# Performance work log

Measured on AMD Instinct MI355X. Metric: run time of the kernel, lower is better.

Reference implementation:

```python
import jax, jax.numpy as jnp
import numpy as np

N_NODES = 100000
N_EDGES = 3200000
NUM_FEAT = 14
DIM = 16
K_HOPS = 2


def setup_inputs() -> dict:
    key = jax.random.key(0)
    k1, k2, k3, k4 = jax.random.split(key, 4)
    x = jax.random.normal(k1, (N_NODES, NUM_FEAT), dtype=jnp.float32)
    edge_index = jax.random.randint(k2, (2, N_EDGES), 0, N_NODES, dtype=jnp.int64)
    # SGConv's final Linear(num_feat, dim): weight [dim, num_feat], bias [dim]
    W = jax.random.normal(k3, (DIM, NUM_FEAT), dtype=jnp.float32) / np.sqrt(NUM_FEAT)
    b = jax.random.normal(k4, (DIM,), dtype=jnp.float32) * 0.01
    return {"x": x, "edge_index": edge_index, "W": W, "b": b}


def reference(x, edge_index, W, b):
    N = x.shape[0]
    # gcn_norm: add self loops, symmetric degree normalization
    loops = jnp.arange(N, dtype=edge_index.dtype)
    row = jnp.concatenate([edge_index[0], loops])  # source nodes
    col = jnp.concatenate([edge_index[1], loops])  # destination nodes
    ones = jnp.ones(row.shape[0], dtype=x.dtype)
    deg = jax.ops.segment_sum(ones, col, num_segments=N)
    dinv = jnp.where(deg > 0, jax.lax.rsqrt(deg), 0.0)
    norm = dinv[row] * dinv[col]  # [E + N]
    # K-hop propagation: x <- (D^-1/2 (A+I) D^-1/2) x, repeated K times
    for _ in range(K_HOPS):
        x = jax.ops.segment_sum(norm[:, None] * x[row], col, num_segments=N)
    # final linear
    return x @ W.T + b
```

## Files before the change

### kernel.cpp

```cpp
#include <hip/hip_runtime.h>
#include <hip/hip_fp16.h>

#define NF 14
#define DIMOUT 16
#define BSH 9
#define NPBKT 512
#define NBKT 256
#define C1 4096
#define GSUB 8

__device__ __forceinline__ bool detect64(const int* e32) {
    bool is64 = true;
#pragma unroll
    for (int i = 1; i < 64; i += 2) is64 &= (e32[i] == 0);
    return is64;
}

__global__ __launch_bounds__(256) void k_lhist(const void* __restrict__ edges,
                                               int* __restrict__ lhistT, int E, int NBLK) {
    __shared__ int h[NBKT];
    const int t = threadIdx.x;
    h[t] = 0;
    __syncthreads();
    const int* e32 = (const int*)edges;
    const long long* e64 = (const long long*)edges;
    const bool is64 = detect64(e32);
    const int base = blockIdx.x * C1;
    const int cnt = min(C1, E - base);
    if (is64) {
        const longlong2* p2 = (const longlong2*)(e64 + (size_t)E + base);
        for (int j = 2 * t; j < cnt; j += 512) {
            longlong2 v = p2[j >> 1];
            atomicAdd(&h[((int)v.x) >> BSH], 1);
            atomicAdd(&h[((int)v.y) >> BSH], 1);
        }
    } else {
        const int2* p2 = (const int2*)(e32 + (size_t)E + base);
        for (int j = 2 * t; j < cnt; j += 512) {
            int2 v = p2[j >> 1];
            atomicAdd(&h[v.x >> BSH], 1);
            atomicAdd(&h[v.y >> BSH], 1);
        }
    }
    __syncthreads();
    lhistT[(size_t)t * NBLK + blockIdx.x] = h[t];
}

__global__ __launch_bounds__(256) void k_cscan(const int* __restrict__ lhistT,
                                               int* __restrict__ lbase,
                                               int* __restrict__ btot, int NBLK) {
    const int b = blockIdx.x;
    const int t = threadIdx.x;
    const int IPT = (NBLK + 255) / 256;
    int v[8];
    int s = 0;
    for (int k = 0; k < IPT; ++k) {
        int j = t * IPT + k;
        int x = (j < NBLK) ? lhistT[(size_t)b * NBLK + j] : 0;
        v[k] = x;
        s += x;
    }
    __shared__ int sm[256];
    sm[t] = s;
    __syncthreads();
    for (int d = 1; d < 256; d <<= 1) {
        int u = (t >= d) ? sm[t - d] : 0;
        __syncthreads();
        sm[t] += u;
        __syncthreads();
    }
    int run = sm[t] - s;
    for (int k = 0; k < IPT; ++k) {
        int j = t * IPT + k;
        if (j < NBLK) {
            lbase[(size_t)b * NBLK + j] = run;
            run += v[k];
        }
    }
    if (t == 255) btot[b] = sm[255];
}

__global__ __launch_bounds__(NBKT) void k_gscan(const int* __restrict__ btot,
                                                int* __restrict__ gregion) {
    __shared__ int sm[NBKT];
    int t = threadIdx.x;
    int v = btot[t];
    sm[t] = v;
    __syncthreads();
    for (int d = 1; d < NBKT; d <<= 1) {
        int u = (t >= d) ? sm[t - d] : 0;
        __syncthreads();
        sm[t] += u;
        __syncthreads();
    }
    gregion[t] = sm[t] - v;
    if (t == NBKT - 1) gregion[NBKT] = sm[t];
}

__global__ __launch_bounds__(256) void k_scatter(const void* __restrict__ edges,
                                                 const int* __restrict__ gregion,
                                                 const int* __restrict__ lbase,
                                                 unsigned int* __restrict__ pairs,
                                                 int E, int NBLK) {
    __shared__ unsigned int raw[C1];
    __shared__ unsigned int srt[C1];
    __shared__ unsigned short bkt[C1];
    __shared__ unsigned char sbk[C1];
    __shared__ int hist[NBKT], scn[NBKT], gb[NBKT], cur[NBKT];
    const int* e32 = (const int*)edges;
    const long long* e64 = (const long long*)edges;
    const bool is64 = detect64(e32);
    const int t = threadIdx.x;
    const int base = blockIdx.x * C1;
    const int cnt = min(C1, E - base);
    hist[t] = 0;
    cur[t] = 0;
    __syncthreads();
    for (int j = 2 * t; j < cnt; j += 512) {
        int s0, s1, d0, d1;
        if (is64) {
            longlong2 vs = *(const longlong2*)(e64 + (size_t)base + j);
            longlong2 vd = *(const longlong2*)(e64 + (size_t)E + base + j);
            s0 = (int)vs.x;
            s1 = (int)vs.y;
            d0 = (int)vd.x;
            d1 = (int)vd.y;
        } else {
            int2 vs = *(const int2*)(e32 + (size_t)base + j);
            int2 vd = *(const int2*)(e32 + (size_t)E + base + j);
            s0 = vs.x;
            s1 = vs.y;
            d0 = vd.x;
            d1 = vd.y;
        }
        int b0 = d0 >> BSH, b1 = d1 >> BSH;
        raw[j] = (unsigned int)s0 | ((unsigned int)(d0 & (NPBKT - 1)) << 17);
        raw[j + 1] = (unsigned int)s1 | ((unsigned int)(d1 & (NPBKT - 1)) << 17);
        bkt[j] = (unsigned short)b0;
        bkt[j + 1] = (unsigned short)b1;
        atomicAdd(&hist[b0], 1);
        atomicAdd(&hist[b1], 1);
    }
    __syncthreads();
    int v = hist[t];
    scn[t] = v;
    __syncthreads();
    for (int d = 1; d < NBKT; d <<= 1) {
        int u = (t >= d) ? scn[t - d] : 0;
        __syncthreads();
        scn[t] += u;
        __syncthreads();
    }
    int ex = scn[t] - v;
    gb[t] = gregion[t] + lbase[(size_t)t * NBLK + blockIdx.x];
    __syncthreads();
    scn[t] = ex;
    __syncthreads();
    for (int j = t; j < cnt; j += 256) {
        int b = bkt[j];
        int r = atomicAdd(&cur[b], 1);
        int pos = scn[b] + r;
        srt[pos] = raw[j];
        sbk[pos] = (unsigned char)b;
    }
    __syncthreads();
    for (int j = t; j < cnt; j += 256) {
        int b = sbk[j];
        pairs[gb[b] + (j - scn[b])] = srt[j];
    }
}

__global__ __launch_bounds__(256) void k_nhist(const unsigned int* __restrict__ pairs,
                                               const int* __restrict__ gregion,
                                               int* __restrict__ nh, int N) {
    const int b = blockIdx.x >> 3;
    const int g = blockIdx.x & 7;
    const int e0 = gregion[b], e1 = gregion[b + 1];
    const int L = e1 - e0;
    const int sb = e0 + ((L * g) >> 3);
    const int se = e0 + ((L * (g + 1)) >> 3);
    __shared__ int h[NPBKT];
    const int t = threadIdx.x;
    h[t] = 0;
    h[t + 256] = 0;
    __syncthreads();
    for (int e = sb + t; e < se; e += 256) atomicAdd(&h[pairs[e] >> 17], 1);
    __syncthreads();
    const int nbase = b << BSH;
    for (int l = t; l < NPBKT; l += 256) {
        int n = nbase + l;
        if (n < N) nh[(size_t)g * N + n] = h[l];
    }
}

__global__ __launch_bounds__(256) void k_nscan(int* __restrict__ nh,
                                               float* __restrict__ dinv,
                                               int2* __restrict__ lc,
                                               int* __restrict__ btot2, int N) {
    const int t = threadIdx.x;
    const int n = blockIdx.x * 256 + t;
    int c = 0, p = 0;
    if (n < N) {
        int v[GSUB];
        int ex = 0;
#pragma unroll
        for (int g = 0; g < GSUB; ++g) v[g] = nh[(size_t)g * N + n];
#pragma unroll
        for (int g = 0; g < GSUB; ++g) {
            int vv = v[g];
            nh[(size_t)g * N + n] = ex;
            ex += vv;
        }
        c = ex;
        p = (c + 8) & ~7;
        dinv[n] = rsqrtf((float)(c + 1));
    }
    __shared__ int sm[256];
    sm[t] = p;
    __syncthreads();
    for (int d = 1; d < 256; d <<= 1) {
        int u = (t >= d) ? sm[t - d] : 0;
        __syncthreads();
        sm[t] += u;
        __syncthreads();
    }
    if (n < N) lc[n] = make_int2(sm[t] - p, c);
    if (t == 255) btot2[blockIdx.x] = sm[255];
}

__global__ __launch_bounds__(512) void k_gscan2(const int* __restrict__ btot2,
                                                int* __restrict__ bbase2, int nb) {
    __shared__ int sm[512];
    int t = threadIdx.x;
    int v = (t < nb) ? btot2[t] : 0;
    sm[t] = v;
    __syncthreads();
    for (int d = 1; d < 512; d <<= 1) {
        int u = (t >= d) ? sm[t - d] : 0;
        __syncthreads();
        sm[t] += u;
        __syncthreads();
    }
    if (t < nb) bbase2[t] = sm[t] - v;
}

__global__ __launch_bounds__(256) void k_nscatter(const unsigned int* __restrict__ pairs,
                                                  const int* __restrict__ gregion,
                                                  const int* __restrict__ nh,
                                                  const int2* __restrict__ lc,
                                                  const int* __restrict__ bbase2,
                                                  int2* __restrict__ off2,
                                                  int* __restrict__ srcs, int N) {
    const int b = blockIdx.x >> 3;
    const int g = blockIdx.x & 7;
    const int e0 = gregion[b], e1 = gregion[b + 1];
    const int L = e1 - e0;
    const int sb = e0 + ((L * g) >> 3);
    const int se = e0 + ((L * (g + 1)) >> 3);
    __shared__ int cur[NPBKT];
    const int t = threadIdx.x;
    const int nbase = b << BSH;
    for (int l = t; l < NPBKT; l += 256) {
        int n = nbase + l;
        if (n < N) {
            int2 lcv = lc[n];
            int off = bbase2[n >> 8] + lcv.x;
            cur[l] = off + 1 + nh[(size_t)g * N + n];
            if (g == 0) {
                int c = lcv.y;
                int p = (c + 8) & ~7;
                off2[n] = make_int2(off, off + p);
                srcs[off] = n;
                for (int k = c + 1; k < p; ++k) srcs[off + k] = N;
            }
        }
    }
    __syncthreads();
    for (int e = sb + t; e < se; e += 256) {
        unsigned int pr = pairs[e];
        int l = pr >> 17;
        int r = atomicAdd(&cur[l], 1);
        srcs[r] = (int)(pr & 0x1FFFFu);
    }
}

__global__ __launch_bounds__(256) void k_prep(const float* __restrict__ x,
                                              const float* __restrict__ dinv,
                                              const float* __restrict__ Wg,
                                              __half2* __restrict__ u0,
                                              __half2* __restrict__ u1, int N) {
    __shared__ float Wl[DIMOUT * NF];
    int t = threadIdx.x;
    if (t < DIMOUT * NF) Wl[t] = Wg[t];
    __syncthreads();
    if (blockIdx.x == 0 && t < 8) {
        u0[(size_t)N * 8 + t] = __floats2half2_rn(0.f, 0.f);
        u1[(size_t)N * 8 + t] = __floats2half2_rn(0.f, 0.f);
    }
    int n = blockIdx.x * 256 + t;
    if (n >= N) return;
    float xr[NF];
    const float2* xr2 = (const float2*)(x + (size_t)n * NF);
#pragma unroll
    for (int k = 0; k < 7; ++k) {
        float2 v = xr2[k];
        xr[2 * k] = v.x;
        xr[2 * k + 1] = v.y;
    }
    float dn = dinv[n];
#pragma unroll
    for (int q = 0; q < 8; ++q) {
        float r0 = 0.f, r1 = 0.f;
#pragma unroll
        for (int f = 0; f < NF; ++f) {
            r0 += xr[f] * Wl[(2 * q) * NF + f];
            r1 += xr[f] * Wl[(2 * q + 1) * NF + f];
        }
        u0[(size_t)n * 8 + q] = __floats2half2_rn(dn * r0, dn * r1);
    }
}

template <int FINAL>
__global__ __launch_bounds__(256) void k_hop(const uint2* __restrict__ u8,
                                             const int* __restrict__ srcs,
                                             const int2* __restrict__ off2,
                                             const float* __restrict__ dinv,
                                             const float* __restrict__ bias,
                                             uint2* __restrict__ outh,
                                             float* __restrict__ outf, int N) {
    const int lane = threadIdx.x & 63;
    const int fp = lane & 3;
    const int ep = (lane >> 2) & 7;
    const int half = lane >> 5;
    const int wid = threadIdx.x >> 6;
    float4 breg = make_float4(0.f, 0.f, 0.f, 0.f);
    if (FINAL) breg = *(const float4*)(bias + 4 * fp);
    const int stride = gridDim.x * 8;
    for (int n0 = blockIdx.x * 8 + wid * 2; n0 < N; n0 += stride) {
        const int n = n0 + half;
        const bool act = (n < N);
        int2 oo = act ? off2[n] : make_int2(0, 0);
        float ax = 0.f, ay = 0.f, az = 0.f, aw = 0.f;
        int e = oo.x + ep;
        for (; e + 8 < oo.y; e += 16) {
            int s0 = srcs[e];
            int s1 = srcs[e + 8];
            uint2 q0 = u8[(size_t)s0 * 4 + fp];
            uint2 q1 = u8[(size_t)s1 * 4 + fp];
            float2 a0 = __half22float2(*(__half2*)&q0.x);
            float2 b0 = __half22float2(*(__half2*)&q0.y);
            float2 a1 = __half22float2(*(__half2*)&q1.x);
            float2 b1 = __half22float2(*(__half2*)&q1.y);
            ax += a0.x + a1.x;
            ay += a0.y + a1.y;
            az += b0.x + b1.x;
            aw += b0.y + b1.y;
        }
        if (e < oo.y) {
            int s0 = srcs[e];
            uint2 q0 = u8[(size_t)s0 * 4 + fp];
            float2 a0 = __half22float2(*(__half2*)&q0.x);
            float2 b0 = __half22float2(*(__half2*)&q0.y);
            ax += a0.x;
            ay += a0.y;
            az += b0.x;
            aw += b0.y;
        }
#pragma unroll
        for (int d = 4; d <= 16; d <<= 1) {
            ax += __shfl_xor(ax, d);
            ay += __shfl_xor(ay, d);
            az += __shfl_xor(az, d);
            aw += __shfl_xor(aw, d);
        }
        if (ep == 0 && act) {
            float dn = dinv[n];
            if (!FINAL) {
                float s = dn * dn;
                __half2 h0 = __floats2half2_rn(s * ax, s * ay);
                __half2 h1 = __floats2half2_rn(s * az, s * aw);
                uint2 q;
                q.x = *(unsigned*)&h0;
                q.y = *(unsigned*)&h1;
                outh[(size_t)n * 4 + fp] = q;
            } else {
                float4 o;
                o.x = dn * ax + breg.x;
                o.y = dn * ay + breg.y;
                o.z = dn * az + breg.z;
                o.w = dn * aw + breg.w;
                *(float4*)(outf + (size_t)n * DIMOUT + 4 * fp) = o;
            }
        }
    }
}

extern "C" void kernel_launch(void* const* d_in, const int* in_sizes, int n_in,
                              void* d_out, int out_size, void* d_ws, size_t ws_size,
                              hipStream_t stream) {
    const float* x = (const float*)d_in[0];
    const void* edges = d_in[1];
    const float* W = (const float*)d_in[2];
    const float* b = (const float*)d_in[3];
    float* out = (float*)d_out;

    const int N = in_sizes[0] / NF;
    const int E = in_sizes[1] / 2;
    const int NBLK = (E + C1 - 1) / C1;
    const int NUSED = (N + NPBKT - 1) >> BSH;
    const int NBLK2 = (N + 255) / 256;

    char* ws = (char*)d_ws;
    size_t o = 0;
    auto alloc = [&](size_t bytes) -> void* {
        o = (o + 255) & ~(size_t)255;
        void* p = ws + o;
        o += bytes;
        return p;
    };
    int* lhistT = (int*)alloc((size_t)NBKT * NBLK * sizeof(int));
    int* lbase = (int*)alloc((size_t)NBKT * NBLK * sizeof(int));
    int* btot = (int*)alloc((size_t)NBKT * sizeof(int));
    int* gregion = (int*)alloc(((size_t)NBKT + 1) * sizeof(int));
    unsigned int* pairs = (unsigned int*)alloc((size_t)E * sizeof(unsigned int));
    int* srcs = (int*)alloc(((size_t)E + (size_t)8 * N + 256) * sizeof(int));
    int* nh = (int*)alloc((size_t)GSUB * N * sizeof(int));
    int2* lc = (int2*)alloc((size_t)N * sizeof(int2));
    int* btot2 = (int*)alloc((size_t)NBLK2 * sizeof(int));
    int* bbase2 = (int*)alloc((size_t)NBLK2 * sizeof(int));
    int2* off2 = (int2*)alloc((size_t)N * sizeof(int2));
    float* dinv = (float*)alloc((size_t)N * sizeof(float));
    __half* u0 = (__half*)alloc((size_t)(N + 1) * 16 * sizeof(__half));
    __half* u1 = (__half*)alloc((size_t)(N + 1) * 16 * sizeof(__half));
    (void)ws_size;
    (void)n_in;
    (void)out_size;

    k_lhist<<<NBLK, 256, 0, stream>>>(edges, lhistT, E, NBLK);
    k_cscan<<<NBKT, 256, 0, stream>>>(lhistT, lbase, btot, NBLK);
    k_gscan<<<1, NBKT, 0, stream>>>(btot, gregion);
    k_scatter<<<NBLK, 256, 0, stream>>>(edges, gregion, lbase, pairs, E, NBLK);
    k_nhist<<<NUSED * GSUB, 256, 0, stream>>>(pairs, gregion, nh, N);
    k_nscan<<<NBLK2, 256, 0, stream>>>(nh, dinv, lc, btot2, N);
    k_prep<<<NBLK2, 256, 0, stream>>>(x, dinv, W, (__half2*)u0, (__half2*)u1, N);
    k_gscan2<<<1, 512, 0, stream>>>(btot2, bbase2, NBLK2);
    k_nscatter<<<NUSED * GSUB, 256, 0, stream>>>(pairs, gregion, nh, lc, bbase2,
                                                 off2, srcs, N);

    k_hop<0><<<2048, 256, 0, stream>>>((const uint2*)u0, srcs, off2, dinv, nullptr,
                                       (uint2*)u1, nullptr, N);
    k_hop<1><<<2048, 256, 0, stream>>>((const uint2*)u1, srcs, off2, dinv, b,
                                       nullptr, out, N);
}
```

Measured before the change: 141.0 us.

## Fuse per-node histogram and scan into half-bucket blocks with LDS-staged CSR placement

Replaces the 8-way subdivided node histogram, separate node scan, and global scatter with per-half-bucket kernels. Each block counts degrees for 256 nodes, scans them locally, and records a block total. A placement kernel then stages the CSR source list in shared memory and writes it out contiguously, falling back to direct global writes when the segment exceeds capacity. This drops one kernel launch and the nh intermediate buffer, and makes the srcs writes coalesced. In exchange each block reads the whole bucket twice and filters by half, and there are fewer blocks, so less parallelism.

Result: faster. 121.3 us (-13.9%).

```diff
diff --git a/kernel.cpp b/kernel.cpp
--- a/kernel.cpp
+++ b/kernel.cpp
@@ -7,7 +7,8 @@
 #define NPBKT 512
 #define NBKT 256
 #define C1 4096
-#define GSUB 8
+#define HNODES 256
+#define SCAP 14336
 
 __device__ __forceinline__ bool detect64(const int* e32) {
     bool is64 = true;
@@ -170,69 +171,50 @@
     }
 }
 
-__global__ __launch_bounds__(256) void k_nhist(const unsigned int* __restrict__ pairs,
-                                               const int* __restrict__ gregion,
-                                               int* __restrict__ nh, int N) {
-    const int b = blockIdx.x >> 3;
-    const int g = blockIdx.x & 7;
+__global__ __launch_bounds__(512) void k_hcount(const unsigned int* __restrict__ pairs,
+                                                const int* __restrict__ gregion,
+                                                float* __restrict__ dinv,
+                                                int2* __restrict__ lc,
+                                                int* __restrict__ htot, int N) {
+    const int bh = blockIdx.x;
+    const int b = bh >> 1, h = bh & 1;
     const int e0 = gregion[b], e1 = gregion[b + 1];
-    const int L = e1 - e0;
-    const int sb = e0 + ((L * g) >> 3);
-    const int se = e0 + ((L * (g + 1)) >> 3);
-    __shared__ int h[NPBKT];
+    __shared__ int cnt[HNODES];
+    __shared__ int sm[HNODES];
     const int t = threadIdx.x;
-    h[t] = 0;
-    h[t + 256] = 0;
-    __syncthreads();
-    for (int e = sb + t; e < se; e += 256) atomicAdd(&h[pairs[e] >> 17], 1);
-    __syncthreads();
-    const int nbase = b << BSH;
-    for (int l = t; l < NPBKT; l += 256) {
-        int n = nbase + l;
-        if (n < N) nh[(size_t)g * N + n] = h[l];
-    }
-}
-
-__global__ __launch_bounds__(256) void k_nscan(int* __restrict__ nh,
-                                               float* __restrict__ dinv,
-                                               int2* __restrict__ lc,
-                                               int* __restrict__ btot2, int N) {
-    const int t = threadIdx.x;
-    const int n = blockIdx.x * 256 + t;
+    if (t < HNODES) cnt[t] = 0;
+    __syncthreads();
+    for (int e = e0 + t; e < e1; e += 512) {
+        int dl = (int)(pairs[e] >> 17);
+        if ((dl >> 8) == h) atomicAdd(&cnt[dl & (HNODES - 1)], 1);
+    }
+    __syncthreads();
+    const int nbase = (b << BSH) + h * HNODES;
     int c = 0, p = 0;
-    if (n < N) {
-        int v[GSUB];
-        int ex = 0;
-#pragma unroll
-        for (int g = 0; g < GSUB; ++g) v[g] = nh[(size_t)g * N + n];
-#pragma unroll
-        for (int g = 0; g < GSUB; ++g) {
-            int vv = v[g];
-            nh[(size_t)g * N + n] = ex;
-            ex += vv;
-        }
-        c = ex;
-        p = (c + 8) & ~7;
-        dinv[n] = rsqrtf((float)(c + 1));
-    }
-    __shared__ int sm[256];
-    sm[t] = p;
-    __syncthreads();
-    for (int d = 1; d < 256; d <<= 1) {
-        int u = (t >= d) ? sm[t - d] : 0;
-        __syncthreads();
-        sm[t] += u;
-        __syncthreads();
-    }
-    if (n < N) lc[n] = make_int2(sm[t] - p, c);
-    if (t == 255) btot2[blockIdx.x] = sm[255];
-}
-
-__global__ __launch_bounds__(512) void k_gscan2(const int* __restrict__ btot2,
-                                                int* __restrict__ bbase2, int nb) {
+    if (t < HNODES) {
+        c = cnt[t];
+        if (nbase + t < N) p = (c + 8) & ~7;
+    }
+    if (t < HNODES) sm[t] = p;
+    __syncthreads();
+    for (int d = 1; d < HNODES; d <<= 1) {
+        int u = (t >= d && t < HNODES) ? sm[t - d] : 0;
+        __syncthreads();
+        if (t < HNODES) sm[t] += u;
+        __syncthreads();
+    }
+    if (t < HNODES && nbase + t < N) {
+        lc[nbase + t] = make_int2(sm[t] - p, c);
+        dinv[nbase + t] = rsqrtf((float)(c + 1));
+    }
+    if (t == 0) htot[bh] = sm[HNODES - 1];
+}
+
+__global__ __launch_bounds__(512) void k_gscan2(const int* __restrict__ htot,
+                                                int* __restrict__ hbase, int nb) {
     __shared__ int sm[512];
     int t = threadIdx.x;
-    int v = (t < nb) ? btot2[t] : 0;
+    int v = (t < nb) ? htot[t] : 0;
     sm[t] = v;
     __syncthreads();
     for (int d = 1; d < 512; d <<= 1) {
@@ -241,46 +223,67 @@
         sm[t] += u;
         __syncthreads();
     }
-    if (t < nb) bbase2[t] = sm[t] - v;
-}
-
-__global__ __launch_bounds__(256) void k_nscatter(const unsigned int* __restrict__ pairs,
-                                                  const int* __restrict__ gregion,
-                                                  const int* __restrict__ nh,
-                                                  const int2* __restrict__ lc,
-                                                  const int* __restrict__ bbase2,
-                                                  int2* __restrict__ off2,
-                                                  int* __restrict__ srcs, int N) {
-    const int b = blockIdx.x >> 3;
-    const int g = blockIdx.x & 7;
+    if (t < nb) hbase[t] = sm[t] - v;
+}
+
+__global__ __launch_bounds__(512) void k_hplace(const unsigned int* __restrict__ pairs,
+                                                const int* __restrict__ gregion,
+                                                const int2* __restrict__ lc,
+                                                const int* __restrict__ hbase,
+                                                const int* __restrict__ htot,
+                                                int2* __restrict__ off2,
+                                                int* __restrict__ srcs, int N) {
+    const int bh = blockIdx.x;
+    const int b = bh >> 1, h = bh & 1;
     const int e0 = gregion[b], e1 = gregion[b + 1];
-    const int L = e1 - e0;
-    const int sb = e0 + ((L * g) >> 3);
-    const int se = e0 + ((L * (g + 1)) >> 3);
-    __shared__ int cur[NPBKT];
+    __shared__ int cur[HNODES];
+    __shared__ unsigned staged[SCAP];
     const int t = threadIdx.x;
-    const int nbase = b << BSH;
-    for (int l = t; l < NPBKT; l += 256) {
-        int n = nbase + l;
+    const int nbase = (b << BSH) + h * HNODES;
+    const int gb = hbase[bh];
+    const int span = htot[bh];
+    const bool fits = (span <= SCAP);
+    if (t < HNODES) {
+        int n = nbase + t;
         if (n < N) {
-            int2 lcv = lc[n];
-            int off = bbase2[n >> 8] + lcv.x;
-            cur[l] = off + 1 + nh[(size_t)g * N + n];
-            if (g == 0) {
-                int c = lcv.y;
-                int p = (c + 8) & ~7;
-                off2[n] = make_int2(off, off + p);
-                srcs[off] = n;
-                for (int k = c + 1; k < p; ++k) srcs[off + k] = N;
+            int2 l = lc[n];
+            int c = l.y;
+            int p = (c + 8) & ~7;
+            off2[n] = make_int2(gb + l.x, gb + l.x + p);
+            if (fits) {
+                cur[t] = l.x + 1;
+                staged[l.x] = (unsigned)n;
+                for (int k = c + 1; k < p; ++k) staged[l.x + k] = (unsigned)N;
+            } else {
+                cur[t] = gb + l.x + 1;
+                srcs[gb + l.x] = n;
+                for (int k = c + 1; k < p; ++k) srcs[gb + l.x + k] = N;
             }
-        }
-    }
-    __syncthreads();
-    for (int e = sb + t; e < se; e += 256) {
-        unsigned int pr = pairs[e];
-        int l = pr >> 17;
-        int r = atomicAdd(&cur[l], 1);
-        srcs[r] = (int)(pr & 0x1FFFFu);
+        } else {
+            cur[t] = 0;
+        }
+    }
+    __syncthreads();
+    if (fits) {
+        for (int e = e0 + t; e < e1; e += 512) {
+            unsigned pr = pairs[e];
+            int dl = (int)(pr >> 17);
+            if ((dl >> 8) == h) {
+                int r = atomicAdd(&cur[dl & (HNODES - 1)], 1);
+                staged[r] = pr & 0x1FFFFu;
+            }
+        }
+        __syncthreads();
+        for (int i = t; i < span; i += 512) srcs[gb + i] = (int)staged[i];
+    } else {
+        for (int e = e0 + t; e < e1; e += 512) {
+            unsigned pr = pairs[e];
+            int dl = (int)(pr >> 17);
+            if ((dl >> 8) == h) {
+                int r = atomicAdd(&cur[dl & (HNODES - 1)], 1);
+                srcs[r] = (int)(pr & 0x1FFFFu);
+            }
+        }
     }
 }
 
@@ -408,7 +411,7 @@
     const int E = in_sizes[1] / 2;
     const int NBLK = (E + C1 - 1) / C1;
     const int NUSED = (N + NPBKT - 1) >> BSH;
-    const int NBLK2 = (N + 255) / 256;
+    const int NBH = NUSED * 2;
 
     char* ws = (char*)d_ws;
     size_t o = 0;
@@ -424,10 +427,9 @@
     int* gregion = (int*)alloc(((size_t)NBKT + 1) * sizeof(int));
     unsigned int* pairs = (unsigned int*)alloc((size_t)E * sizeof(unsigned int));
     int* srcs = (int*)alloc(((size_t)E + (size_t)8 * N + 256) * sizeof(int));
-    int* nh = (int*)alloc((size_t)GSUB * N * sizeof(int));
     int2* lc = (int2*)alloc((size_t)N * sizeof(int2));
-    int* btot2 = (int*)alloc((size_t)NBLK2 * sizeof(int));
-    int* bbase2 = (int*)alloc((size_t)NBLK2 * sizeof(int));
+    int* htot = (int*)alloc((size_t)NBH * sizeof(int));
+    int* hbase = (int*)alloc((size_t)NBH * sizeof(int));
     int2* off2 = (int2*)alloc((size_t)N * sizeof(int2));
     float* dinv = (float*)alloc((size_t)N * sizeof(float));
     __half* u0 = (__half*)alloc((size_t)(N + 1) * 16 * sizeof(__half));
@@ -440,12 +442,11 @@
     k_cscan<<<NBKT, 256, 0, stream>>>(lhistT, lbase, btot, NBLK);
     k_gscan<<<1, NBKT, 0, stream>>>(btot, gregion);
     k_scatter<<<NBLK, 256, 0, stream>>>(edges, gregion, lbase, pairs, E, NBLK);
-    k_nhist<<<NUSED * GSUB, 256, 0, stream>>>(pairs, gregion, nh, N);
-    k_nscan<<<NBLK2, 256, 0, stream>>>(nh, dinv, lc, btot2, N);
-    k_prep<<<NBLK2, 256, 0, stream>>>(x, dinv, W, (__half2*)u0, (__half2*)u1, N);
-    k_gscan2<<<1, 512, 0, stream>>>(btot2, bbase2, NBLK2);
-    k_nscatter<<<NUSED * GSUB, 256, 0, stream>>>(pairs, gregion, nh, lc, bbase2,
-                                                 off2, srcs, N);
+    k_hcount<<<NBH, 512, 0, stream>>>(pairs, gregion, dinv, lc, htot, N);
+    k_gscan2<<<1, 512, 0, stream>>>(htot, hbase, NBH);
+    k_prep<<<(N + 255) / 256, 256, 0, stream>>>(x, dinv, W, (__half2*)u0,
+                                                (__half2*)u1, N);
+    k_hplace<<<NBH, 512, 0, stream>>>(pairs, gregion, lc, hbase, htot, off2, srcs, N);
 
     k_hop<0><<<2048, 256, 0, stream>>>((const uint2*)u0, srcs, off2, dinv, nullptr,
                                        (uint2*)u1, nullptr, N);
```
